# Optimization experiments

Hardware: AMD Instinct MI355X
Metric: run time of the kernel (lower is better)

Reference implementation:

```python
import jax, jax.numpy as jnp
import numpy as np

NT = 3            # node types
NET = 9           # edge types = all ordered pairs
PAIR_A = np.repeat(np.arange(NT), NT)   # et[0].value per edge type
PAIR_B = np.tile(np.arange(NT), NT)     # et[1].value per edge type


def setup_inputs() -> dict:
    key = jax.random.key(0)
    ks = jax.random.split(key, 20)
    bs, Na, Nc, CS, D, H, Z = 8, 128, 256, 3, 64, 64, 8
    s = 0.05
    inp = {
        'node_types': jax.random.randint(ks[0], (bs, Na), 0, NT),
        'node_enc': jax.random.normal(ks[1], (bs, Na, D), dtype=jnp.float32),
        'edge_enc': jax.random.normal(ks[2], (bs, Na, Na, 1, D), dtype=jnp.float32),
        'clique_index': jax.random.randint(ks[3], (bs, Nc), 0, Na),
        'clique_node_index': jax.random.randint(ks[4], (bs, Nc, CS), 0, Na),
        'clique_order_index': jax.random.randint(ks[5], (bs, Nc, CS), 0, CS),
        # per-node-type MLP params (stacked over type axis)
        'nW0': jax.random.normal(ks[6], (NT, D, H)) * s, 'nb0': jnp.zeros((NT, H)),
        'nW1': jax.random.normal(ks[7], (NT, H, H)) * s, 'nb1': jnp.zeros((NT, H)),
        'nW2': jax.random.normal(ks[8], (NT, H, Z)) * s, 'nb2': jnp.zeros((NT, Z)),
        # per-edge-type MLP params
        'eW0': jax.random.normal(ks[9], (NET, D, H)) * s, 'eb0': jnp.zeros((NET, H)),
        'eW1': jax.random.normal(ks[10], (NET, H, H)) * s, 'eb1': jnp.zeros((NET, H)),
        'eW2': jax.random.normal(ks[11], (NET, H, Z * Z)) * s, 'eb2': jnp.zeros((NET, Z * Z)),
    }
    return inp


def reference(node_types, node_enc, edge_enc, clique_index, clique_node_index,
              clique_order_index, nW0, nb0, nW1, nb1, nW2, nb2,
              eW0, eb0, eW1, eb1, eW2, eb2):
    bs, Na = node_types.shape
    Nc, cs = clique_node_index.shape[1:]
    Z = nb2.shape[-1]

    # ---- node factors: dense per-type MLP then type-mask accumulate ----
    h = jax.nn.relu(jnp.einsum('bnd,tdh->tbnh', node_enc, nW0) + nb0[:, None, None, :])
    h = jax.nn.relu(jnp.einsum('tbnh,thk->tbnk', h, nW1) + nb1[:, None, None, :])
    nf_all = jnp.einsum('tbnk,tkz->tbnz', h, nW2) + nb2[:, None, None, :]  # [T,bs,Na,Z]
    nmask = (node_types[None] == jnp.arange(NT)[:, None, None]).astype(nf_all.dtype)
    node_factor = jnp.einsum('tbnz,tbn->bnz', nf_all, nmask)  # [bs,Na,Z]

    # ---- edge factors: last timestep of edge_enc, per-pair-type MLP + mask ----
    e = edge_enc[..., -1, :]  # [bs,Na,Na,D]
    h = jax.nn.relu(jnp.einsum('bijd,tdh->tbijh', e, eW0) + eb0[:, None, None, None, :])
    h = jax.nn.relu(jnp.einsum('tbijh,thk->tbijk', h, eW1) + eb1[:, None, None, None, :])
    ef_all = jnp.einsum('tbijk,tkz->tbijz', h, eW2) + eb2[:, None, None, None, :]  # [9,bs,Na,Na,Z*Z]
    pa = jnp.asarray(PAIR_A)
    pb = jnp.asarray(PAIR_B)
    # et_flag[b,i,j] = (types[b,j]==et0) & (types[b,i]==et1)  (matches torch unsqueeze(1)/(2))
    emask = ((node_types[None, :, None, :] == pa[:, None, None, None]) &
             (node_types[None, :, :, None] == pb[:, None, None, None])).astype(ef_all.dtype)
    edge_factor = jnp.einsum('tbijz,tbij->bijz', ef_all, emask).reshape(bs, Na, Na, Z, Z)

    # ---- pad with zero row/col for index -1 sentinel ----
    nfe = jnp.pad(node_factor, ((0, 0), (0, 1), (0, 0)))                     # [bs,Na+1,Z]
    efe = jnp.pad(edge_factor, ((0, 0), (0, 1), (0, 1), (0, 0), (0, 0)))
    efe_flat = efe.reshape(bs, (Na + 1) * (Na + 1), Z, Z)

    idx = jnp.where(clique_node_index < 0, Na, clique_node_index)  # [bs,Nc,cs]
    b_ix = jnp.arange(bs)[:, None, None]
    nfc = nfe[b_ix, idx]  # [bs,Nc,cs,Z]

    logpi = jnp.zeros((bs, Nc) + (Z,) * cs, node_factor.dtype)
    for i in range(cs):
        shape = (bs, Nc) + (1,) * i + (Z,) + (1,) * (cs - 1 - i)
        logpi = logpi + nfc[:, :, i, :].reshape(shape)
    b2 = jnp.arange(bs)[:, None]
    for i in range(cs - 1):
        for j in range(i + 1, cs):
            fl = idx[:, :, i] * (Na + 1) + idx[:, :, j]          # [bs,Nc]
            ef_ij = efe_flat[b2, fl]                              # [bs,Nc,Z,Z]
            shape = (bs, Nc) + (1,) * i + (Z,) + (1,) * (j - i - 1) + (Z,) + (1,) * (cs - 1 - j)
            logpi = logpi + ef_ij.reshape(shape)

    z = jnp.stack(jnp.meshgrid(*([jnp.arange(Z)] * cs), indexing='ij'), -1)
    return logpi, z
```

## Files before the change

kernel.cpp:

```cpp
#include <hip/hip_runtime.h>
#include <hip/hip_bf16.h>


#define BS   8
#define NA   128
#define NC   256
#define DIM  64
#define ZZ   8

__global__ __launch_bounds__(64) void node_mlp_kernel(
    const int* __restrict__ nt, const float* __restrict__ enc,
    const float* __restrict__ W0, const float* __restrict__ b0,
    const float* __restrict__ W1, const float* __restrict__ b1,
    const float* __restrict__ W2, const float* __restrict__ b2,
    float* __restrict__ nf ) {
  const int blk  = blockIdx.x;
  const int lane = threadIdx.x;
  const int t = nt[blk];

  __shared__ float e[DIM];
  __shared__ float h[DIM];

  e[lane] = enc[blk * DIM + lane];
  __syncthreads();

  float acc = b0[t * DIM + lane];
  {
    const float* w = W0 + t * DIM * DIM;
#pragma unroll
    for (int d = 0; d < DIM; ++d) acc = fmaf(e[d], w[d * DIM + lane], acc);
  }
  acc = fmaxf(acc, 0.f);
  h[lane] = acc;
  __syncthreads();

  acc = b1[t * DIM + lane];
  {
    const float* w = W1 + t * DIM * DIM;
#pragma unroll
    for (int d = 0; d < DIM; ++d) acc = fmaf(h[d], w[d * DIM + lane], acc);
  }
  acc = fmaxf(acc, 0.f);
  __syncthreads();
  e[lane] = acc;
  __syncthreads();

  if (lane < ZZ) {
    float a2 = b2[t * ZZ + lane];
    const float* w2 = W2 + t * DIM * ZZ;
#pragma unroll
    for (int k = 0; k < DIM; ++k) a2 = fmaf(e[k], w2[k * ZZ + lane], a2);
    nf[blk * ZZ + lane] = a2;
  }
}

__global__ __launch_bounds__(64) void clique_kernel(
    const int* __restrict__ nt, const int* __restrict__ cni,
    const float* __restrict__ edge_enc, const float* __restrict__ nf,
    const float* __restrict__ eW0, const float* __restrict__ eb0,
    const float* __restrict__ eW1, const float* __restrict__ eb1,
    const float* __restrict__ eW2, const float* __restrict__ eb2,
    float* __restrict__ out) {
  const int blk  = blockIdx.x;
  const int lane = threadIdx.x;
  const int b = blk >> 8;

  __shared__ float e[DIM];
  __shared__ float h[DIM];
  __shared__ float nfs[3][ZZ];
  __shared__ float ef[3][DIM];
  __shared__ int   idxs[3];

  if (lane < 3) {
    int v = cni[blk * 3 + lane];
    if (v < 0 || v >= NA) v = NA;
    idxs[lane] = v;
  }
  __syncthreads();

  if (lane < 3 * ZZ) {
    const int i = lane >> 3, z = lane & 7;
    const int v = idxs[i];
    nfs[i][z] = (v < NA) ? nf[(b * NA + v) * ZZ + z] : 0.f;
  }

  const int pi[3] = {0, 0, 1};
  const int pj[3] = {1, 2, 2};

  for (int p = 0; p < 3; ++p) {
    const int ia = idxs[pi[p]];
    const int jb = idxs[pj[p]];
    if (ia >= NA || jb >= NA) {
      ef[p][lane] = 0.f;
      continue;
    }
    const int t = nt[b * NA + jb] * 3 + nt[b * NA + ia];

    __syncthreads();
    e[lane] = edge_enc[((b * NA + ia) * NA + jb) * DIM + lane];
    __syncthreads();

    float acc = eb0[t * DIM + lane];
    {
      const float* w = eW0 + t * DIM * DIM;
#pragma unroll
      for (int d = 0; d < DIM; ++d) acc = fmaf(e[d], w[d * DIM + lane], acc);
    }
    acc = fmaxf(acc, 0.f);
    h[lane] = acc;
    __syncthreads();

    acc = eb1[t * DIM + lane];
    {
      const float* w = eW1 + t * DIM * DIM;
#pragma unroll
      for (int d = 0; d < DIM; ++d) acc = fmaf(h[d], w[d * DIM + lane], acc);
    }
    acc = fmaxf(acc, 0.f);
    __syncthreads();
    e[lane] = acc;
    __syncthreads();

    acc = eb2[t * DIM + lane];
    {
      const float* w = eW2 + t * DIM * DIM;
#pragma unroll
      for (int d = 0; d < DIM; ++d) acc = fmaf(e[d], w[d * DIM + lane], acc);
    }
    ef[p][lane] = acc;
  }
  __syncthreads();

  const int z1 = lane >> 3, z2 = lane & 7;
  const float base = nfs[1][z1] + nfs[2][z2] + ef[2][z1 * ZZ + z2];
  float* o = out + blk * (ZZ * ZZ * ZZ);
#pragma unroll
  for (int z0 = 0; z0 < ZZ; ++z0) {
    o[z0 * 64 + lane] = base + nfs[0][z0] + ef[0][z0 * ZZ + z1] + ef[1][z0 * ZZ + z2];
  }
}

__global__ __launch_bounds__(256) void z_kernel(float* __restrict__ out) {
  const int i = blockIdx.x * 256 + threadIdx.x;
  if (i < ZZ * ZZ * ZZ * 3) {
    const int k = i % 3;
    const int r = i / 3;
    const int z2 = r & 7, z1 = (r >> 3) & 7, z0 = r >> 6;
    const int v = (k == 0) ? z0 : ((k == 1) ? z1 : z2);
    out[BS * NC * ZZ * ZZ * ZZ + i] = (float)v;
  }
}

extern "C" void kernel_launch(void* const* d_in, const int* in_sizes, int n_in,
                              void* d_out, int out_size, void* d_ws, size_t ws_size,
                              hipStream_t stream) {
  const int*   node_types = (const int*)  d_in[0];
  const float* node_enc   = (const float*)d_in[1];
  const float* edge_enc   = (const float*)d_in[2];
  const int*   cni        = (const int*)  d_in[4];
  const float* nW0 = (const float*)d_in[6];
  const float* nb0 = (const float*)d_in[7];
  const float* nW1 = (const float*)d_in[8];
  const float* nb1 = (const float*)d_in[9];
  const float* nW2 = (const float*)d_in[10];
  const float* nb2 = (const float*)d_in[11];
  const float* eW0 = (const float*)d_in[12];
  const float* eb0 = (const float*)d_in[13];
  const float* eW1 = (const float*)d_in[14];
  const float* eb1 = (const float*)d_in[15];
  const float* eW2 = (const float*)d_in[16];
  const float* eb2 = (const float*)d_in[17];

  float* out = (float*)d_out;
  float* node_factor = (float*)d_ws;

  node_mlp_kernel<<<BS * NA, 64, 0, stream>>>(
      node_types, node_enc, nW0, nb0, nW1, nb1, nW2, nb2, node_factor);

  clique_kernel<<<BS * NC, 64, 0, stream>>>(
      node_types, cni, edge_enc, node_factor,
      eW0, eb0, eW1, eb1, eW2, eb2, out);

  z_kernel<<<(ZZ * ZZ * ZZ * 3 + 255) / 256, 256, 0, stream>>>(out);
}
```

Before: 126.8 us.

## Split clique kernel into per-edge MLP and assemble kernels with split-K

The fused clique kernel, which ran three serial edge MLPs per 64-thread block, is split into an edge MLP kernel that runs one block per (clique, pair) and an assemble kernel that reads the edge factors back from workspace. Each MLP layer now uses 256 threads with a 4-way split-K and a shared-memory reduction, in both the node and edge kernels. The z-grid fill is folded into the assemble kernel, so one launch is dropped. This trades a workspace round trip, extra syncs and one more kernel boundary for more parallelism and a shorter dependent FMA chain per thread.

```diff
diff --git a/kernel.cpp b/kernel.cpp
--- a/kernel.cpp
+++ b/kernel.cpp
@@ -8,127 +8,176 @@
 #define DIM  64
 #define ZZ   8
 
-__global__ __launch_bounds__(64) void node_mlp_kernel(
+#define WS_EF_OFF (BS * NA * ZZ)
+
+__global__ __launch_bounds__(256) void node_mlp_kernel(
     const int* __restrict__ nt, const float* __restrict__ enc,
     const float* __restrict__ W0, const float* __restrict__ b0,
     const float* __restrict__ W1, const float* __restrict__ b1,
     const float* __restrict__ W2, const float* __restrict__ b2,
-    float* __restrict__ nf ) {
-  const int blk  = blockIdx.x;
-  const int lane = threadIdx.x;
+    float* __restrict__ nf) {
+  const int blk = blockIdx.x;
+  const int tid = threadIdx.x;
+  const int j = tid & 63, s = tid >> 6;
   const int t = nt[blk];
 
   __shared__ float e[DIM];
   __shared__ float h[DIM];
-
-  e[lane] = enc[blk * DIM + lane];
-  __syncthreads();
-
-  float acc = b0[t * DIM + lane];
-  {
-    const float* w = W0 + t * DIM * DIM;
-#pragma unroll
-    for (int d = 0; d < DIM; ++d) acc = fmaf(e[d], w[d * DIM + lane], acc);
-  }
-  acc = fmaxf(acc, 0.f);
-  h[lane] = acc;
-  __syncthreads();
-
-  acc = b1[t * DIM + lane];
-  {
-    const float* w = W1 + t * DIM * DIM;
-#pragma unroll
-    for (int d = 0; d < DIM; ++d) acc = fmaf(h[d], w[d * DIM + lane], acc);
-  }
-  acc = fmaxf(acc, 0.f);
-  __syncthreads();
-  e[lane] = acc;
-  __syncthreads();
-
-  if (lane < ZZ) {
-    float a2 = b2[t * ZZ + lane];
-    const float* w2 = W2 + t * DIM * ZZ;
-#pragma unroll
-    for (int k = 0; k < DIM; ++k) a2 = fmaf(e[k], w2[k * ZZ + lane], a2);
-    nf[blk * ZZ + lane] = a2;
-  }
-}
-
-__global__ __launch_bounds__(64) void clique_kernel(
+  __shared__ float red[4][DIM];
+  __shared__ float red2[8][ZZ];
+
+  if (tid < DIM) e[tid] = enc[blk * DIM + tid];
+  __syncthreads();
+
+  {
+    float a = 0.f;
+    const float* w = W0 + t * DIM * DIM + s * 16 * DIM + j;
+#pragma unroll
+    for (int k = 0; k < 16; ++k) a = fmaf(e[s * 16 + k], w[k * DIM], a);
+    red[s][j] = a;
+  }
+  __syncthreads();
+  if (s == 0) {
+    float v = red[0][j] + red[1][j] + red[2][j] + red[3][j] + b0[t * DIM + j];
+    h[j] = fmaxf(v, 0.f);
+  }
+  __syncthreads();
+
+  {
+    float a = 0.f;
+    const float* w = W1 + t * DIM * DIM + s * 16 * DIM + j;
+#pragma unroll
+    for (int k = 0; k < 16; ++k) a = fmaf(h[s * 16 + k], w[k * DIM], a);
+    red[s][j] = a;
+  }
+  __syncthreads();
+  if (s == 0) {
+    float v = red[0][j] + red[1][j] + red[2][j] + red[3][j] + b1[t * DIM + j];
+    e[j] = fmaxf(v, 0.f);
+  }
+  __syncthreads();
+
+  if (tid < DIM) {
+    const int j2 = tid & 7, s2 = tid >> 3;
+    float a = 0.f;
+    const float* w = W2 + t * DIM * ZZ + s2 * 8 * ZZ + j2;
+#pragma unroll
+    for (int k = 0; k < 8; ++k) a = fmaf(e[s2 * 8 + k], w[k * ZZ], a);
+    red2[s2][j2] = a;
+  }
+  __syncthreads();
+  if (tid < ZZ) {
+    float v = b2[t * ZZ + tid];
+#pragma unroll
+    for (int s2 = 0; s2 < 8; ++s2) v += red2[s2][tid];
+    nf[blk * ZZ + tid] = v;
+  }
+}
+
+__global__ __launch_bounds__(256) void edge_mlp_kernel(
     const int* __restrict__ nt, const int* __restrict__ cni,
-    const float* __restrict__ edge_enc, const float* __restrict__ nf,
+    const float* __restrict__ edge_enc,
     const float* __restrict__ eW0, const float* __restrict__ eb0,
     const float* __restrict__ eW1, const float* __restrict__ eb1,
     const float* __restrict__ eW2, const float* __restrict__ eb2,
-    float* __restrict__ out) {
-  const int blk  = blockIdx.x;
+    float* __restrict__ ef_out) {
+  const int blk = blockIdx.x;
+  const int tid = threadIdx.x;
+  const int j = tid & 63, s = tid >> 6;
+  const int clique = blk / 3, pair = blk - clique * 3;
+  const int b = clique >> 8;
+
+  const int pi = (pair == 2) ? 1 : 0;
+  const int pj = (pair == 0) ? 1 : 2;
+
+  __shared__ int idxs[2];
+  __shared__ float e[DIM];
+  __shared__ float h[DIM];
+  __shared__ float red[4][DIM];
+
+  if (tid == 0) {
+    int va = cni[clique * 3 + pi];
+    int vb = cni[clique * 3 + pj];
+    idxs[0] = (va < 0 || va >= NA) ? NA : va;
+    idxs[1] = (vb < 0 || vb >= NA) ? NA : vb;
+  }
+  __syncthreads();
+  const int ia = idxs[0], jb = idxs[1];
+
+  if (ia >= NA || jb >= NA) {
+    if (tid < DIM) ef_out[blk * DIM + tid] = 0.f;
+    return;
+  }
+  const int t = nt[b * NA + jb] * 3 + nt[b * NA + ia];
+
+  if (tid < DIM) e[tid] = edge_enc[((b * NA + ia) * NA + jb) * DIM + tid];
+  __syncthreads();
+
+  {
+    float a = 0.f;
+    const float* w = eW0 + t * DIM * DIM + s * 16 * DIM + j;
+#pragma unroll
+    for (int k = 0; k < 16; ++k) a = fmaf(e[s * 16 + k], w[k * DIM], a);
+    red[s][j] = a;
+  }
+  __syncthreads();
+  if (s == 0) {
+    float v = red[0][j] + red[1][j] + red[2][j] + red[3][j] + eb0[t * DIM + j];
+    h[j] = fmaxf(v, 0.f);
+  }
+  __syncthreads();
+
+  {
+    float a = 0.f;
+    const float* w = eW1 + t * DIM * DIM + s * 16 * DIM + j;
+#pragma unroll
+    for (int k = 0; k < 16; ++k) a = fmaf(h[s * 16 + k], w[k * DIM], a);
+    red[s][j] = a;
+  }
+  __syncthreads();
+  if (s == 0) {
+    float v = red[0][j] + red[1][j] + red[2][j] + red[3][j] + eb1[t * DIM + j];
+    e[j] = fmaxf(v, 0.f);
+  }
+  __syncthreads();
+
+  {
+    float a = 0.f;
+    const float* w = eW2 + t * DIM * DIM + s * 16 * DIM + j;
+#pragma unroll
+    for (int k = 0; k < 16; ++k) a = fmaf(e[s * 16 + k], w[k * DIM], a);
+    red[s][j] = a;
+  }
+  __syncthreads();
+  if (s == 0) {
+    ef_out[blk * DIM + j] =
+        red[0][j] + red[1][j] + red[2][j] + red[3][j] + eb2[t * DIM + j];
+  }
+}
+
+__global__ __launch_bounds__(64) void assemble_kernel(
+    const int* __restrict__ cni, const float* __restrict__ nf,
+    const float* __restrict__ ef_in, float* __restrict__ out) {
+  const int blk = blockIdx.x;
   const int lane = threadIdx.x;
   const int b = blk >> 8;
 
-  __shared__ float e[DIM];
-  __shared__ float h[DIM];
+  __shared__ int idxs[3];
   __shared__ float nfs[3][ZZ];
   __shared__ float ef[3][DIM];
-  __shared__ int   idxs[3];
 
   if (lane < 3) {
     int v = cni[blk * 3 + lane];
-    if (v < 0 || v >= NA) v = NA;
-    idxs[lane] = v;
-  }
-  __syncthreads();
-
+    idxs[lane] = (v < 0 || v >= NA) ? NA : v;
+  }
+  __syncthreads();
   if (lane < 3 * ZZ) {
     const int i = lane >> 3, z = lane & 7;
     const int v = idxs[i];
     nfs[i][z] = (v < NA) ? nf[(b * NA + v) * ZZ + z] : 0.f;
   }
-
-  const int pi[3] = {0, 0, 1};
-  const int pj[3] = {1, 2, 2};
-
-  for (int p = 0; p < 3; ++p) {
-    const int ia = idxs[pi[p]];
-    const int jb = idxs[pj[p]];
-    if (ia >= NA || jb >= NA) {
-      ef[p][lane] = 0.f;
-      continue;
-    }
-    const int t = nt[b * NA + jb] * 3 + nt[b * NA + ia];
-
-    __syncthreads();
-    e[lane] = edge_enc[((b * NA + ia) * NA + jb) * DIM + lane];
-    __syncthreads();
-
-    float acc = eb0[t * DIM + lane];
-    {
-      const float* w = eW0 + t * DIM * DIM;
-#pragma unroll
-      for (int d = 0; d < DIM; ++d) acc = fmaf(e[d], w[d * DIM + lane], acc);
-    }
-    acc = fmaxf(acc, 0.f);
-    h[lane] = acc;
-    __syncthreads();
-
-    acc = eb1[t * DIM + lane];
-    {
-      const float* w = eW1 + t * DIM * DIM;
-#pragma unroll
-      for (int d = 0; d < DIM; ++d) acc = fmaf(h[d], w[d * DIM + lane], acc);
-    }
-    acc = fmaxf(acc, 0.f);
-    __syncthreads();
-    e[lane] = acc;
-    __syncthreads();
-
-    acc = eb2[t * DIM + lane];
-    {
-      const float* w = eW2 + t * DIM * DIM;
-#pragma unroll
-      for (int d = 0; d < DIM; ++d) acc = fmaf(e[d], w[d * DIM + lane], acc);
-    }
-    ef[p][lane] = acc;
-  }
+#pragma unroll
+  for (int p = 0; p < 3; ++p) ef[p][lane] = ef_in[(blk * 3 + p) * DIM + lane];
   __syncthreads();
 
   const int z1 = lane >> 3, z2 = lane & 7;
@@ -138,15 +187,13 @@
   for (int z0 = 0; z0 < ZZ; ++z0) {
     o[z0 * 64 + lane] = base + nfs[0][z0] + ef[0][z0 * ZZ + z1] + ef[1][z0 * ZZ + z2];
   }
-}
-
-__global__ __launch_bounds__(256) void z_kernel(float* __restrict__ out) {
-  const int i = blockIdx.x * 256 + threadIdx.x;
-  if (i < ZZ * ZZ * ZZ * 3) {
+
+  if (blk < 24) {
+    const int i = blk * 64 + lane;
     const int k = i % 3;
     const int r = i / 3;
-    const int z2 = r & 7, z1 = (r >> 3) & 7, z0 = r >> 6;
-    const int v = (k == 0) ? z0 : ((k == 1) ? z1 : z2);
+    const int zz2 = r & 7, zz1 = (r >> 3) & 7, zz0 = r >> 6;
+    const int v = (k == 0) ? zz0 : ((k == 1) ? zz1 : zz2);
     out[BS * NC * ZZ * ZZ * ZZ + i] = (float)v;
   }
 }
@@ -173,13 +220,13 @@
 
   float* out = (float*)d_out;
   float* node_factor = (float*)d_ws;
-
-  node_mlp_kernel<<<BS * NA, 64, 0, stream>>>(
+  float* ef_buf = (float*)d_ws + WS_EF_OFF;
+
+  node_mlp_kernel<<<BS * NA, 256, 0, stream>>>(
       node_types, node_enc, nW0, nb0, nW1, nb1, nW2, nb2, node_factor);
 
-  clique_kernel<<<BS * NC, 64, 0, stream>>>(
-      node_types, cni, edge_enc, node_factor,
-      eW0, eb0, eW1, eb1, eW2, eb2, out);
-
-  z_kernel<<<(ZZ * ZZ * ZZ * 3 + 255) / 256, 256, 0, stream>>>(out);
-}
+  edge_mlp_kernel<<<BS * NC * 3, 256, 0, stream>>>(
+      node_types, cni, edge_enc, eW0, eb0, eW1, eb1, eW2, eb2, ef_buf);
+
+  assemble_kernel<<<BS * NC, 64, 0, stream>>>(cni, node_factor, ef_buf, out);
+}
```

Result: no change. 125.7 us, median of 2 (-0.8%).

## Run clique edge MLPs on parallel waves with shuffles, fuse z output

Applied to the files above, without the earlier changes.

The clique kernel becomes a 256-thread block in which three waves each evaluate one edge-pair MLP concurrently and a fourth wave gathers the node factors, replacing the serial three-pass loop. Activations are broadcast with __shfl instead of shared memory plus barriers, and the node MLP gets the same treatment, with its last layer split across all lanes and reduced by xor shuffles. The separate z-grid kernel is folded into the clique kernel, removing one launch. The cost is more threads per block, with waves that sit idle in the output phase.

```diff
diff --git a/kernel.cpp b/kernel.cpp
--- a/kernel.cpp
+++ b/kernel.cpp
@@ -18,43 +18,39 @@
   const int lane = threadIdx.x;
   const int t = nt[blk];
 
-  __shared__ float e[DIM];
-  __shared__ float h[DIM];
-
-  e[lane] = enc[blk * DIM + lane];
-  __syncthreads();
+  float e = enc[blk * DIM + lane];
 
   float acc = b0[t * DIM + lane];
   {
-    const float* w = W0 + t * DIM * DIM;
+    const float* w = W0 + t * DIM * DIM + lane;
 #pragma unroll
-    for (int d = 0; d < DIM; ++d) acc = fmaf(e[d], w[d * DIM + lane], acc);
+    for (int k = 0; k < DIM; ++k) acc = fmaf(__shfl(e, k), w[k * DIM], acc);
   }
-  acc = fmaxf(acc, 0.f);
-  h[lane] = acc;
-  __syncthreads();
+  float h = fmaxf(acc, 0.f);
 
   acc = b1[t * DIM + lane];
   {
-    const float* w = W1 + t * DIM * DIM;
+    const float* w = W1 + t * DIM * DIM + lane;
 #pragma unroll
-    for (int d = 0; d < DIM; ++d) acc = fmaf(h[d], w[d * DIM + lane], acc);
+    for (int k = 0; k < DIM; ++k) acc = fmaf(__shfl(h, k), w[k * DIM], acc);
   }
-  acc = fmaxf(acc, 0.f);
-  __syncthreads();
-  e[lane] = acc;
-  __syncthreads();
+  float h1 = fmaxf(acc, 0.f);
 
-  if (lane < ZZ) {
-    float a2 = b2[t * ZZ + lane];
-    const float* w2 = W2 + t * DIM * ZZ;
+  const int z = lane & 7, s = lane >> 3;
+  acc = 0.f;
+  {
+    const float* w2 = W2 + t * DIM * ZZ + z;
 #pragma unroll
-    for (int k = 0; k < DIM; ++k) a2 = fmaf(e[k], w2[k * ZZ + lane], a2);
-    nf[blk * ZZ + lane] = a2;
+    for (int k = 0; k < 8; ++k)
+      acc = fmaf(__shfl(h1, s * 8 + k), w2[(s * 8 + k) * ZZ], acc);
   }
+  acc += __shfl_xor(acc, 8);
+  acc += __shfl_xor(acc, 16);
+  acc += __shfl_xor(acc, 32);
+  if (lane < ZZ) nf[blk * ZZ + lane] = acc + b2[t * ZZ + lane];
 }
 
-__global__ __launch_bounds__(64) void clique_kernel(
+__global__ __launch_bounds__(256) void clique_fused_kernel(
     const int* __restrict__ nt, const int* __restrict__ cni,
     const float* __restrict__ edge_enc, const float* __restrict__ nf,
     const float* __restrict__ eW0, const float* __restrict__ eb0,
@@ -62,91 +58,77 @@
     const float* __restrict__ eW2, const float* __restrict__ eb2,
     float* __restrict__ out) {
   const int blk  = blockIdx.x;
-  const int lane = threadIdx.x;
+  const int tid  = threadIdx.x;
+  const int wave = tid >> 6, lane = tid & 63;
   const int b = blk >> 8;
 
-  __shared__ float e[DIM];
-  __shared__ float h[DIM];
+  __shared__ int   idxs[3];
   __shared__ float nfs[3][ZZ];
   __shared__ float ef[3][DIM];
-  __shared__ int   idxs[3];
 
-  if (lane < 3) {
-    int v = cni[blk * 3 + lane];
-    if (v < 0 || v >= NA) v = NA;
-    idxs[lane] = v;
+  if (tid < 3) {
+    int v = cni[blk * 3 + tid];
+    idxs[tid] = (v < 0 || v >= NA) ? NA : v;
   }
   __syncthreads();
 
-  if (lane < 3 * ZZ) {
-    const int i = lane >> 3, z = lane & 7;
-    const int v = idxs[i];
-    nfs[i][z] = (v < NA) ? nf[(b * NA + v) * ZZ + z] : 0.f;
-  }
-
-  const int pi[3] = {0, 0, 1};
-  const int pj[3] = {1, 2, 2};
-
-  for (int p = 0; p < 3; ++p) {
-    const int ia = idxs[pi[p]];
-    const int jb = idxs[pj[p]];
+  if (wave == 3) {
+    if (lane < 3 * ZZ) {
+      const int i = lane >> 3, z = lane & 7, v = idxs[i];
+      nfs[i][z] = (v < NA) ? nf[(b * NA + v) * ZZ + z] : 0.f;
+    }
+  } else {
+    const int p = wave;
+    const int pi = (p == 2) ? 1 : 0;
+    const int pj = (p == 0) ? 1 : 2;
+    const int ia = idxs[pi], jb = idxs[pj];
     if (ia >= NA || jb >= NA) {
       ef[p][lane] = 0.f;
-      continue;
+    } else {
+      const int t = nt[b * NA + jb] * 3 + nt[b * NA + ia];
+      float e = edge_enc[((b * NA + ia) * NA + jb) * DIM + lane];
+
+      float acc = eb0[t * DIM + lane];
+      {
+        const float* w = eW0 + t * DIM * DIM + lane;
+#pragma unroll
+        for (int k = 0; k < DIM; ++k) acc = fmaf(__shfl(e, k), w[k * DIM], acc);
+      }
+      e = fmaxf(acc, 0.f);
+
+      acc = eb1[t * DIM + lane];
+      {
+        const float* w = eW1 + t * DIM * DIM + lane;
+#pragma unroll
+        for (int k = 0; k < DIM; ++k) acc = fmaf(__shfl(e, k), w[k * DIM], acc);
+      }
+      e = fmaxf(acc, 0.f);
+
+      acc = eb2[t * DIM + lane];
+      {
+        const float* w = eW2 + t * DIM * DIM + lane;
+#pragma unroll
+        for (int k = 0; k < DIM; ++k) acc = fmaf(__shfl(e, k), w[k * DIM], acc);
+      }
+      ef[p][lane] = acc;
     }
-    const int t = nt[b * NA + jb] * 3 + nt[b * NA + ia];
-
-    __syncthreads();
-    e[lane] = edge_enc[((b * NA + ia) * NA + jb) * DIM + lane];
-    __syncthreads();
-
-    float acc = eb0[t * DIM + lane];
-    {
-      const float* w = eW0 + t * DIM * DIM;
-#pragma unroll
-      for (int d = 0; d < DIM; ++d) acc = fmaf(e[d], w[d * DIM + lane], acc);
-    }
-    acc = fmaxf(acc, 0.f);
-    h[lane] = acc;
-    __syncthreads();
-
-    acc = eb1[t * DIM + lane];
-    {
-      const float* w = eW1 + t * DIM * DIM;
-#pragma unroll
-      for (int d = 0; d < DIM; ++d) acc = fmaf(h[d], w[d * DIM + lane], acc);
-    }
-    acc = fmaxf(acc, 0.f);
-    __syncthreads();
-    e[lane] = acc;
-    __syncthreads();
-
-    acc = eb2[t * DIM + lane];
-    {
-      const float* w = eW2 + t * DIM * DIM;
-#pragma unroll
-      for (int d = 0; d < DIM; ++d) acc = fmaf(e[d], w[d * DIM + lane], acc);
-    }
-    ef[p][lane] = acc;
   }
   __syncthreads();
 
-  const int z1 = lane >> 3, z2 = lane & 7;
-  const float base = nfs[1][z1] + nfs[2][z2] + ef[2][z1 * ZZ + z2];
-  float* o = out + blk * (ZZ * ZZ * ZZ);
+  if (wave == 0) {
+    const int z1 = lane >> 3, z2 = lane & 7;
+    const float base = nfs[1][z1] + nfs[2][z2] + ef[2][z1 * ZZ + z2];
+    float* o = out + blk * (ZZ * ZZ * ZZ);
 #pragma unroll
-  for (int z0 = 0; z0 < ZZ; ++z0) {
-    o[z0 * 64 + lane] = base + nfs[0][z0] + ef[0][z0 * ZZ + z1] + ef[1][z0 * ZZ + z2];
-  }
-}
-
-__global__ __launch_bounds__(256) void z_kernel(float* __restrict__ out) {
-  const int i = blockIdx.x * 256 + threadIdx.x;
-  if (i < ZZ * ZZ * ZZ * 3) {
+    for (int z0 = 0; z0 < ZZ; ++z0) {
+      o[z0 * 64 + lane] = base + nfs[0][z0] + ef[0][z0 * ZZ + z1] + ef[1][z0 * ZZ + z2];
+    }
+  } else if (wave == 1 && blk < 24) {
+    const int i = blk * 64 + lane;
     const int k = i % 3;
     const int r = i / 3;
-    const int z2 = r & 7, z1 = (r >> 3) & 7, z0 = r >> 6;
-    const int v = (k == 0) ? z0 : ((k == 1) ? z1 : z2);
+    const int zz2 = r & 7, zz1 = (r >> 3) & 7, zz0 = r >> 6;
+    const int v = (k == 0) ? zz0 : ((k == 1) ? zz1 : zz2);
     out[BS * NC * ZZ * ZZ * ZZ + i] = (float)v;
   }
 }
@@ -177,9 +159,7 @@
   node_mlp_kernel<<<BS * NA, 64, 0, stream>>>(
       node_types, node_enc, nW0, nb0, nW1, nb1, nW2, nb2, node_factor);
 
-  clique_kernel<<<BS * NC, 64, 0, stream>>>(
+  clique_fused_kernel<<<BS * NC, 256, 0, stream>>>(
       node_types, cni, edge_enc, node_factor,
       eW0, eb0, eW1, eb1, eW2, eb2, out);
-
-  z_kernel<<<(ZZ * ZZ * ZZ * 3 + 255) / 256, 256, 0, stream>>>(out);
 }
```

After: 128.0 us. Within noise of the previous version (+1.0%).
